# Performance work log

Measured on AMD Instinct MI355X. Metric: run time of the kernel, lower is better.

The kernel has to match this reference:

```python
import jax, jax.numpy as jnp
import numpy as np

G, M, K = 4096, 50, 30          # graphs, nodes per graph, sort-pool k
H, NUM_LAYERS, F_IN = 32, 3, 128
DEG = 8
N = G * M
E = N * DEG
D_LAT = H * NUM_LAYERS + 1       # 97 = conv1d kernel/stride
DENSE_DIM = (((K - 2) // 2 + 1) - 5 + 1) * 32  # 352


def setup_inputs() -> dict:
    key = jax.random.key(0)
    ks = jax.random.split(key, 14)
    x = jax.random.normal(ks[0], (N, F_IN), dtype=jnp.float32)
    # graph-local random edges so each subgraph is self-contained
    offs = (jnp.arange(E, dtype=jnp.int32) // (M * DEG)) * M
    src = jax.random.randint(ks[1], (E,), 0, M, dtype=jnp.int32) + offs
    dst = jax.random.randint(ks[2], (E,), 0, M, dtype=jnp.int32) + offs
    edge_index = jnp.stack([src, dst])
    batch = jnp.repeat(jnp.arange(G, dtype=jnp.int32), M)

    def lin(k, i, o):
        return (jax.random.normal(k, (i, o), dtype=jnp.float32) / np.sqrt(i)).astype(jnp.float32)

    W0, b0 = lin(ks[3], F_IN, H), jnp.zeros((H,), jnp.float32)
    W1, b1 = lin(ks[4], H, H), jnp.zeros((H,), jnp.float32)
    W2, b2 = lin(ks[5], H, H), jnp.zeros((H,), jnp.float32)
    W3, b3 = lin(ks[6], H, 1), jnp.zeros((1,), jnp.float32)
    C1w = (jax.random.normal(ks[7], (16, 1, D_LAT)) / np.sqrt(D_LAT)).astype(jnp.float32)
    C1b = jnp.zeros((16,), jnp.float32)
    C2w = (jax.random.normal(ks[8], (32, 16, 5)) / np.sqrt(16 * 5)).astype(jnp.float32)
    C2b = jnp.zeros((32,), jnp.float32)
    L1w, L1b = lin(ks[9], DENSE_DIM, 128), jnp.zeros((128,), jnp.float32)
    L2w, L2b = lin(ks[10], 128, 1), jnp.zeros((1,), jnp.float32)
    return {"x": x, "edge_index": edge_index, "batch": batch,
            "W0": W0, "b0": b0, "W1": W1, "b1": b1, "W2": W2, "b2": b2,
            "W3": W3, "b3": b3, "C1w": C1w, "C1b": C1b, "C2w": C2w, "C2b": C2b,
            "L1w": L1w, "L1b": L1b, "L2w": L2w, "L2b": L2b}


def _gcn_norm(edge_index, n):
    # add self loops, symmetric normalization (PyG GCNConv default)
    loop = jnp.arange(n, dtype=edge_index.dtype)
    src = jnp.concatenate([edge_index[0], loop])
    dst = jnp.concatenate([edge_index[1], loop])
    deg = jax.ops.segment_sum(jnp.ones_like(dst, dtype=jnp.float32), dst, num_segments=n)
    dinv = jnp.where(deg > 0, deg ** -0.5, 0.0)
    return src, dst, dinv[src] * dinv[dst]


def _gcn_conv(h, W, b, src, dst, norm, n):
    h = h @ W                                    # [N, out]
    msg = h[src] * norm[:, None]                 # gather + weight
    return jax.ops.segment_sum(msg, dst, num_segments=n) + b


def reference(x, edge_index, batch, W0, b0, W1, b1, W2, b2, W3, b3,
              C1w, C1b, C2w, C2b, L1w, L1b, L2w, L2b):
    n = x.shape[0]
    src, dst, norm = _gcn_norm(edge_index, n)
    h1 = jnp.tanh(_gcn_conv(x, W0, b0, src, dst, norm, n))
    h2 = jnp.tanh(_gcn_conv(h1, W1, b1, src, dst, norm, n))
    h3 = jnp.tanh(_gcn_conv(h2, W2, b2, src, dst, norm, n))
    h4 = jnp.tanh(_gcn_conv(h3, W3, b3, src, dst, norm, n))
    lat = jnp.concatenate([h1, h2, h3, h4], axis=-1)      # [N, 97]
    # global_sort_pool: graphs are contiguous equal-size blocks (batch = arange(G).repeat(M)),
    # sort nodes within each graph by last channel, descending, keep top K
    xd = lat.reshape(G, M, D_LAT)
    order = jnp.argsort(-xd[..., -1], axis=1)             # [G, M]
    xs = jnp.take_along_axis(xd, order[..., None], axis=1)[:, :K]  # [G, K, 97]
    # Conv1d(1,16,97,stride=97) on [G,1,K*97] == per-slot linear over the 97 latent dims
    z = jnp.einsum('gtd,cd->gct', xs, C1w[:, 0, :]) + C1b[None, :, None]  # [G,16,K]
    z = jax.nn.relu(z)
    z = z.reshape(G, 16, K // 2, 2).max(axis=-1)          # MaxPool1d(2,2) -> [G,16,15]
    z = jax.lax.conv_general_dilated(z, C2w, window_strides=(1,), padding='VALID',
                                     dimension_numbers=('NCH', 'OIH', 'NCH'))
    z = jax.nn.relu(z + C2b[None, :, None])               # [G,32,11]
    z = z.reshape(G, -1)                                  # [G,352]
    z = jax.nn.relu(z @ L1w + L1b)
    # dropout: eval mode (identity)
    return z @ L2w + L2b                                  # [G,1]
```

## Files before the change

kernel.cpp:

```cpp
#include <hip/hip_runtime.h>
#include <math.h>

#define NG 4096
#define M 50
#define KTOP 30
#define H 32
#define F_IN 128
#define EPG 400
#define PADE 552
#define E_TOTAL (NG * EPG)
#define DLAT 97
#define LATS 100
#define NTHREADS 256
#define WS_C1P 0
#define XH 64

__device__ __forceinline__ float fast_tanh(float x) {
    x = fminf(fmaxf(x, -15.f), 15.f);
    float e = __expf(2.f * x);
    return 1.f - 2.f / (e + 1.f);
}

__global__ void prep_kernel(const float* __restrict__ C1w, float* __restrict__ ws) {
    const int tid = blockIdx.x * blockDim.x + threadIdx.x;
    if (tid < 1600) {
        int c = tid / 100, d = tid - c * 100;
        ws[WS_C1P + tid] = (d < DLAT) ? C1w[c * DLAT + d] : 0.f;
    }
}

template <int KIN>
__device__ __forceinline__ void gcn_matmul_acc(const float* hin, int istride,
                                               const float* W,
                                               const int* rows, float* acc, int j) {
#pragma unroll 2
    for (int k4 = 0; k4 < KIN / 4; k4++) {
        const float w0 = W[(4 * k4 + 0) * H + j];
        const float w1 = W[(4 * k4 + 1) * H + j];
        const float w2 = W[(4 * k4 + 2) * H + j];
        const float w3 = W[(4 * k4 + 3) * H + j];
#pragma unroll
        for (int r = 0; r < 7; r++) {
            const float4 xv = *(const float4*)(hin + rows[r] * istride + 4 * k4);
            acc[r] += xv.x * w0 + xv.y * w1 + xv.z * w2 + xv.w * w3;
        }
    }
}

template <int KIN>
__device__ __forceinline__ void gcn_matmul(const float* hin, int istride,
                                           const float* W,
                                           float (*tb)[H], const float* dinv, int tid) {
    const int j = tid & 31, iset = tid >> 5;
    float acc[7];
    int rows[7];
#pragma unroll
    for (int r = 0; r < 7; r++) {
        acc[r] = 0.f;
        int i = iset + r * 8;
        rows[r] = (i >= M) ? (M - 1) : i;
    }
    gcn_matmul_acc<KIN>(hin, istride, W, rows, acc, j);
#pragma unroll
    for (int r = 0; r < 7; r++) {
        int i = iset + r * 8;
        if (i < M) tb[i][j] = acc[r] * dinv[i];
    }
}

__device__ __forceinline__ void gcn_agg(const float (*tbuf)[H], const float* __restrict__ b,
                                        float (*lat)[LATS], int col0,
                                        const float* dinv, const unsigned short* csr_off,
                                        const unsigned char* csr_src, int tid) {
    const int j = tid & 31, iset = tid >> 5;
    for (int i = iset; i < M; i += 8) {
        float acc = tbuf[i][j];
        int e0 = csr_off[i], e1 = csr_off[i + 1];
        for (int e = e0; e < e1; e += 4) {
            unsigned sp = *(const unsigned*)(csr_src + e);
            acc += tbuf[sp & 255][j];
            acc += tbuf[(sp >> 8) & 255][j];
            acc += tbuf[(sp >> 16) & 255][j];
            acc += tbuf[sp >> 24][j];
        }
        lat[i][col0 + j] = fast_tanh(acc * dinv[i] + b[j]);
    }
}

struct Post {
    float pbuf[16][15];
    union {
        struct { float z1[16][KTOP]; unsigned char ord[52]; } a;
        struct { float z2[352]; float red[256]; } b;
    } u;
};

__global__ __launch_bounds__(NTHREADS, 4)
void dgcnn_kernel(const float* __restrict__ x, const int* __restrict__ eidx,
                  const float* __restrict__ ws,
                  const float* __restrict__ W0, const float* __restrict__ b0,
                  const float* __restrict__ W1, const float* __restrict__ b1,
                  const float* __restrict__ W2, const float* __restrict__ b2,
                  const float* __restrict__ W3, const float* __restrict__ b3,
                  const float* __restrict__ C1b,
                  const float* __restrict__ C2w, const float* __restrict__ C2b,
                  const float* __restrict__ L1w, const float* __restrict__ L1b,
                  const float* __restrict__ L2w, const float* __restrict__ L2b,
                  float* __restrict__ out) {
    __shared__ __align__(16) union Big {
        struct { float xs[M][XH]; float w0h[XH][H]; } p1;
        float lat[M][LATS];
    } big;
    __shared__ __align__(16) union TP {
        float tbuf[M + 1][H];
        Post post;
    } tp;
    __shared__ __align__(16) union W12U {
        float w[2][H][H];
        float c2w[32 * 16 * 5];
    } w12u;
    __shared__ unsigned char csr_src[PADE];
    __shared__ unsigned short csr_off[M + 2];
    __shared__ int   degi[M];
    __shared__ float dinv[M];

    const int g = blockIdx.x;
    const int tid = threadIdx.x;
    const int nbase = g * M;
    const int ebase = g * EPG;

    {
        const float4* xg4 = (const float4*)(x + (size_t)nbase * F_IN);
        float4* xs4 = (float4*)big.p1.xs;
        for (int idx = tid; idx < M * XH / 4; idx += NTHREADS) {
            int i = idx >> 4, q = idx & 15;
            xs4[idx] = xg4[i * 32 + q];
        }
        float4* w0f = (float4*)big.p1.w0h;
        const float4* w0g = (const float4*)W0;
        for (int idx = tid; idx < 512; idx += NTHREADS)
            w0f[idx] = w0g[idx];
        float4* wf = (float4*)w12u.w;
        for (int idx = tid; idx < 512; idx += NTHREADS) {
            const float4* srcp = (idx < 256) ? ((const float4*)W1 + idx)
                                             : ((const float4*)W2 + (idx - 256));
            wf[idx] = *srcp;
        }
    }
    if (tid < M) degi[tid] = 1;
    for (int idx = tid; idx < PADE / 4; idx += NTHREADS)
        ((unsigned*)csr_src)[idx] = 0x32323232u;
    __syncthreads();
    for (int e = tid; e < EPG; e += NTHREADS) {
        int d = eidx[E_TOTAL + ebase + e] - nbase;
        atomicAdd(&degi[d], 1);
    }
    __syncthreads();
    if (tid < M) dinv[tid] = rsqrtf((float)degi[tid]);
    if (tid < 64) {
        int cnt  = (tid < M) ? (degi[tid] - 1) : 0;
        int cntp = (cnt + 3) & ~3;
        int incl = cntp;
#pragma unroll
        for (int off = 1; off < 64; off <<= 1) {
            int nv = __shfl_up(incl, off);
            if (tid >= off) incl += nv;
        }
        if (tid < M) {
            csr_off[tid] = (unsigned short)(incl - cntp);
            degi[tid] = incl - cntp;
        }
        if (tid == M - 1) csr_off[M] = (unsigned short)incl;
    }
    __syncthreads();
    const int j1 = tid & 31, iset1 = tid >> 5;
    float acc1[7];
    int rows1[7];
#pragma unroll
    for (int r = 0; r < 7; r++) {
        acc1[r] = 0.f;
        int i = iset1 + r * 8;
        rows1[r] = (i >= M) ? (M - 1) : i;
    }
    for (int e = tid; e < EPG; e += NTHREADS) {
        int s = eidx[ebase + e] - nbase;
        int d = eidx[E_TOTAL + ebase + e] - nbase;
        int pos = atomicAdd(&degi[d], 1);
        csr_src[pos] = (unsigned char)s;
    }
    gcn_matmul_acc<XH>(&big.p1.xs[0][0], XH, &big.p1.w0h[0][0], rows1, acc1, j1);
    __syncthreads();
    {
        const float4* xg4 = (const float4*)(x + (size_t)nbase * F_IN);
        float4* xs4 = (float4*)big.p1.xs;
        for (int idx = tid; idx < M * XH / 4; idx += NTHREADS) {
            int i = idx >> 4, q = idx & 15;
            xs4[idx] = xg4[i * 32 + 16 + q];
        }
        float4* w0f = (float4*)big.p1.w0h;
        const float4* w0g = (const float4*)(W0 + XH * H);
        for (int idx = tid; idx < 512; idx += NTHREADS)
            w0f[idx] = w0g[idx];
    }
    __syncthreads();
    gcn_matmul_acc<XH>(&big.p1.xs[0][0], XH, &big.p1.w0h[0][0], rows1, acc1, j1);
#pragma unroll
    for (int r = 0; r < 7; r++) {
        int i = iset1 + r * 8;
        if (i < M) tp.tbuf[i][j1] = acc1[r] * dinv[i];
    }
    if (tid < H) tp.tbuf[M][tid] = 0.f;
    __syncthreads();

    gcn_agg(tp.tbuf, b0, big.lat, 0, dinv, csr_off, csr_src, tid);
    for (int idx = tid; idx < 3 * M; idx += NTHREADS)
        big.lat[idx / 3][DLAT + idx % 3] = 0.f;
    __syncthreads();
    gcn_matmul<H>(&big.lat[0][0], LATS, &w12u.w[0][0][0], tp.tbuf, dinv, tid);
    __syncthreads();
    gcn_agg(tp.tbuf, b1, big.lat, 32, dinv, csr_off, csr_src, tid);
    __syncthreads();
    gcn_matmul<H>(&big.lat[0][32], LATS, &w12u.w[1][0][0], tp.tbuf, dinv, tid);
    __syncthreads();
    gcn_agg(tp.tbuf, b2, big.lat, 64, dinv, csr_off, csr_src, tid);
    {
        float4* cf = (float4*)w12u.c2w;
        const float4* cg = (const float4*)C2w;
        for (int idx = tid; idx < 640; idx += NTHREADS)
            cf[idx] = cg[idx];
    }
    __syncthreads();
    if (tid < M) {
        float acc = 0.f;
        for (int k = 0; k < H; k++) acc += big.lat[tid][64 + k] * W3[k];
        tp.tbuf[tid][0] = acc * dinv[tid];
    }
    __syncthreads();
    if (tid < M) {
        float acc = tp.tbuf[tid][0];
        int e0 = csr_off[tid], e1 = csr_off[tid + 1];
        for (int e = e0; e < e1; e += 4) {
            unsigned sp = *(const unsigned*)(csr_src + e);
            acc += tp.tbuf[sp & 255][0] + tp.tbuf[(sp >> 8) & 255][0]
                 + tp.tbuf[(sp >> 16) & 255][0] + tp.tbuf[sp >> 24][0];
        }
        big.lat[tid][96] = tanhf(acc * dinv[tid] + b3[0]);
    }
    __syncthreads();

    if (tid < M) {
        float v = big.lat[tid][96];
        int r = 0;
        for (int jj = 0; jj < M; jj++) {
            float vj = big.lat[jj][96];
            r += (vj > v) || (vj == v && jj < tid);
        }
        tp.post.u.a.ord[r] = (unsigned char)tid;
    }
    __syncthreads();

    for (int idx = tid; idx < 16 * KTOP; idx += NTHREADS) {
        int t = idx >> 4, c = idx & 15;
        const float4* row = (const float4*)big.lat[tp.post.u.a.ord[t]];
        const float4* cw  = (const float4*)(ws + WS_C1P + c * LATS);
        float acc = 0.f;
#pragma unroll 5
        for (int q = 0; q < LATS / 4; q++) {
            float4 rv = row[q], wv = cw[q];
            acc += rv.x * wv.x + rv.y * wv.y + rv.z * wv.z + rv.w * wv.w;
        }
        tp.post.u.a.z1[c][t] = fmaxf(acc + C1b[c], 0.f);
    }
    __syncthreads();

    for (int idx = tid; idx < 16 * 15; idx += NTHREADS) {
        int c = idx / 15, t = idx - c * 15;
        tp.post.pbuf[c][t] = fmaxf(tp.post.u.a.z1[c][2 * t],
                                   tp.post.u.a.z1[c][2 * t + 1]);
    }
    __syncthreads();

    for (int idx = tid; idx < 352; idx += NTHREADS) {
        int o = idx / 11, t = idx - o * 11;
        float acc = C2b[o];
        for (int i = 0; i < 16; i++) {
#pragma unroll
            for (int k = 0; k < 5; k++)
                acc += tp.post.pbuf[i][t + k] * w12u.c2w[(o * 16 + i) * 5 + k];
        }
        tp.post.u.b.z2[idx] = fmaxf(acc, 0.f);
    }
    __syncthreads();

    {
        int jj = tid & 127, half = tid >> 7;
        int f0 = half * 176;
        const float* Lp = L1w + (size_t)f0 * 128 + jj;
        const float* zp = tp.post.u.b.z2 + f0;
        float a0 = 0.f, a1 = 0.f, a2 = 0.f, a3 = 0.f;
#pragma unroll 2
        for (int f = 0; f < 176; f += 4) {
            a0 += zp[f]     * Lp[(f)     * 128];
            a1 += zp[f + 1] * Lp[(f + 1) * 128];
            a2 += zp[f + 2] * Lp[(f + 2) * 128];
            a3 += zp[f + 3] * Lp[(f + 3) * 128];
        }
        float acc = (a0 + a1) + (a2 + a3) + ((half == 0) ? L1b[jj] : 0.f);
        tp.post.u.b.red[tid] = acc;
    }
    __syncthreads();
    if (tid < 128)
        tp.post.u.b.red[tid] =
            fmaxf(tp.post.u.b.red[tid] + tp.post.u.b.red[tid + 128], 0.f)
            * L2w[tid];
    __syncthreads();
    if (tid < 64) {
        float v = tp.post.u.b.red[tid] + tp.post.u.b.red[tid + 64];
#pragma unroll
        for (int off = 32; off >= 1; off >>= 1)
            v += __shfl_down(v, off);
        if (tid == 0) out[g] = v + L2b[0];
    }
}

extern "C" void kernel_launch(void* const* d_in, const int* in_sizes, int n_in,
                              void* d_out, int out_size, void* d_ws, size_t ws_size,
                              hipStream_t stream) {
    const float* x    = (const float*)d_in[0];
    const int*   eidx = (const int*)d_in[1];
    float* ws = (float*)d_ws;
    prep_kernel<<<7, 256, 0, stream>>>((const float*)d_in[11], ws);
    dgcnn_kernel<<<NG, NTHREADS, 0, stream>>>(
        x, eidx, ws,
        (const float*)d_in[3],  (const float*)d_in[4],
        (const float*)d_in[5],  (const float*)d_in[6],
        (const float*)d_in[7],  (const float*)d_in[8],
        (const float*)d_in[9],  (const float*)d_in[10],
        (const float*)d_in[12],
        (const float*)d_in[13], (const float*)d_in[14],
        (const float*)d_in[15], (const float*)d_in[16],
        (const float*)d_in[17], (const float*)d_in[18],
        (float*)d_out);
}
```

Measured before the change: 361.4 us.

## Widen CSR gather to 8-byte packs, split accumulators, relax launch bounds

CSR neighbor lists are now padded to multiples of 8 and read as 64-bit words, with two independent accumulators in the aggregation loops. The conv2 loop is also split into two accumulator chains, the matmul unroll goes from 2 to 4, and launch bounds drop from 4 to 2 blocks per SM so the compiler may use more registers. The aim is more instruction-level parallelism and fewer LDS index loads. The cost is more padded edges (extra dummy gathers), more shared memory, and possibly lower occupancy.

```diff
diff --git a/kernel.cpp b/kernel.cpp
--- a/kernel.cpp
+++ b/kernel.cpp
@@ -7,7 +7,7 @@
 #define H 32
 #define F_IN 128
 #define EPG 400
-#define PADE 552
+#define PADE 768
 #define E_TOTAL (NG * EPG)
 #define DLAT 97
 #define LATS 100
@@ -33,7 +33,7 @@
 __device__ __forceinline__ void gcn_matmul_acc(const float* hin, int istride,
                                                const float* W,
                                                const int* rows, float* acc, int j) {
-#pragma unroll 2
+#pragma unroll 4
     for (int k4 = 0; k4 < KIN / 4; k4++) {
         const float w0 = W[(4 * k4 + 0) * H + j];
         const float w1 = W[(4 * k4 + 1) * H + j];
@@ -75,15 +75,20 @@
     const int j = tid & 31, iset = tid >> 5;
     for (int i = iset; i < M; i += 8) {
         float acc = tbuf[i][j];
+        float acc2 = 0.f;
         int e0 = csr_off[i], e1 = csr_off[i + 1];
-        for (int e = e0; e < e1; e += 4) {
-            unsigned sp = *(const unsigned*)(csr_src + e);
-            acc += tbuf[sp & 255][j];
-            acc += tbuf[(sp >> 8) & 255][j];
-            acc += tbuf[(sp >> 16) & 255][j];
-            acc += tbuf[sp >> 24][j];
-        }
-        lat[i][col0 + j] = fast_tanh(acc * dinv[i] + b[j]);
+        for (int e = e0; e < e1; e += 8) {
+            const unsigned long long sp = *(const unsigned long long*)(csr_src + e);
+            acc  += tbuf[(unsigned)(sp)       & 255][j];
+            acc  += tbuf[(unsigned)(sp >> 8)  & 255][j];
+            acc  += tbuf[(unsigned)(sp >> 16) & 255][j];
+            acc  += tbuf[(unsigned)(sp >> 24) & 255][j];
+            acc2 += tbuf[(unsigned)(sp >> 32) & 255][j];
+            acc2 += tbuf[(unsigned)(sp >> 40) & 255][j];
+            acc2 += tbuf[(unsigned)(sp >> 48) & 255][j];
+            acc2 += tbuf[(unsigned)(sp >> 56)      ][j];
+        }
+        lat[i][col0 + j] = fast_tanh((acc + acc2) * dinv[i] + b[j]);
     }
 }
 
@@ -95,7 +100,7 @@
     } u;
 };
 
-__global__ __launch_bounds__(NTHREADS, 4)
+__global__ __launch_bounds__(NTHREADS, 2)
 void dgcnn_kernel(const float* __restrict__ x, const int* __restrict__ eidx,
                   const float* __restrict__ ws,
                   const float* __restrict__ W0, const float* __restrict__ b0,
@@ -119,7 +124,7 @@
         float w[2][H][H];
         float c2w[32 * 16 * 5];
     } w12u;
-    __shared__ unsigned char csr_src[PADE];
+    __shared__ __align__(8) unsigned char csr_src[PADE];
     __shared__ unsigned short csr_off[M + 2];
     __shared__ int   degi[M];
     __shared__ float dinv[M];
@@ -159,7 +164,7 @@
     if (tid < M) dinv[tid] = rsqrtf((float)degi[tid]);
     if (tid < 64) {
         int cnt  = (tid < M) ? (degi[tid] - 1) : 0;
-        int cntp = (cnt + 3) & ~3;
+        int cntp = (cnt + 7) & ~7;
         int incl = cntp;
 #pragma unroll
         for (int off = 1; off < 64; off <<= 1) {
@@ -237,14 +242,20 @@
     }
     __syncthreads();
     if (tid < M) {
-        float acc = tp.tbuf[tid][0];
+        float acc = tp.tbuf[tid][0], acc2 = 0.f;
         int e0 = csr_off[tid], e1 = csr_off[tid + 1];
-        for (int e = e0; e < e1; e += 4) {
-            unsigned sp = *(const unsigned*)(csr_src + e);
-            acc += tp.tbuf[sp & 255][0] + tp.tbuf[(sp >> 8) & 255][0]
-                 + tp.tbuf[(sp >> 16) & 255][0] + tp.tbuf[sp >> 24][0];
-        }
-        big.lat[tid][96] = tanhf(acc * dinv[tid] + b3[0]);
+        for (int e = e0; e < e1; e += 8) {
+            const unsigned long long sp = *(const unsigned long long*)(csr_src + e);
+            acc  += tp.tbuf[(unsigned)(sp)       & 255][0]
+                  + tp.tbuf[(unsigned)(sp >> 8)  & 255][0]
+                  + tp.tbuf[(unsigned)(sp >> 16) & 255][0]
+                  + tp.tbuf[(unsigned)(sp >> 24) & 255][0];
+            acc2 += tp.tbuf[(unsigned)(sp >> 32) & 255][0]
+                  + tp.tbuf[(unsigned)(sp >> 40) & 255][0]
+                  + tp.tbuf[(unsigned)(sp >> 48) & 255][0]
+                  + tp.tbuf[(unsigned)(sp >> 56)      ][0];
+        }
+        big.lat[tid][96] = tanhf((acc + acc2) * dinv[tid] + b3[0]);
     }
     __syncthreads();
 
@@ -282,13 +293,15 @@
 
     for (int idx = tid; idx < 352; idx += NTHREADS) {
         int o = idx / 11, t = idx - o * 11;
-        float acc = C2b[o];
-        for (int i = 0; i < 16; i++) {
-#pragma unroll
-            for (int k = 0; k < 5; k++)
-                acc += tp.post.pbuf[i][t + k] * w12u.c2w[(o * 16 + i) * 5 + k];
-        }
-        tp.post.u.b.z2[idx] = fmaxf(acc, 0.f);
+        float a0 = C2b[o], a1 = 0.f;
+        for (int i = 0; i < 16; i += 2) {
+#pragma unroll
+            for (int k = 0; k < 5; k++) {
+                a0 += tp.post.pbuf[i][t + k]     * w12u.c2w[(o * 16 + i) * 5 + k];
+                a1 += tp.post.pbuf[i + 1][t + k] * w12u.c2w[(o * 16 + i + 1) * 5 + k];
+            }
+        }
+        tp.post.u.b.z2[idx] = fmaxf(a0 + a1, 0.f);
     }
     __syncthreads();
 
```

Measured after the change: 405.6 us. +12.2%, slower.
